# Performance work log

Hardware: AMD Instinct MI355X
Metric: run time of the kernel (lower is better)

## Reference

```python
import jax, jax.numpy as jnp
import numpy as np

N, HID, EMB, T_ENC, T_DEC = 10000, 64, 64, 12, 12


def setup_inputs() -> dict:
    key = jax.random.key(0)
    ks = jax.random.split(key, 16)
    s = 0.05  # small init scale (xavier-ish)
    inputs = jax.random.normal(ks[0], (N, T_ENC), dtype=jnp.float32)
    targets = jax.random.normal(ks[1], (N, T_DEC), dtype=jnp.float32)
    a = jax.random.uniform(ks[2], (N, N), dtype=jnp.float32)
    adj_matrix = a / a.sum(axis=1, keepdims=True)  # row-normalized dense learned adjacency
    D_e = EMB + HID  # encoder cell input dim (embedded input + hidden)
    D_d = 1 + HID    # decoder cell input dim (scalar input + hidden)
    return {
        "inputs": inputs,
        "targets": targets,
        "adj_matrix": adj_matrix,
        "W_emb": jax.random.normal(ks[3], (1, EMB)) * s,
        "b_emb": jnp.full((EMB,), 0.1, dtype=jnp.float32),
        "Wg_e": jax.random.normal(ks[4], (3 * D_e, 2 * HID)) * s,
        "bg_e": jnp.zeros((2 * HID,), jnp.float32),
        "Wc_e": jax.random.normal(ks[5], (3 * D_e, HID)) * s,
        "bc_e": jnp.zeros((HID,), jnp.float32),
        "Wg_d": jax.random.normal(ks[6], (3 * D_d, 2 * HID)) * s,
        "bg_d": jnp.zeros((2 * HID,), jnp.float32),
        "Wc_d": jax.random.normal(ks[7], (3 * D_d, HID)) * s,
        "bc_d": jnp.zeros((HID,), jnp.float32),
        "W_pred": jax.random.normal(ks[8], (HID, 1)) * s,
        "b_pred": jnp.full((1,), 0.1, dtype=jnp.float32),
    }


def _gconv(adj, inp, W, b):
    # Chebyshev-style diffusion with max_diffusion_step = 2: [x0, A x0, 2A(A x0) - x0]
    x1 = adj @ inp
    x2 = 2.0 * (adj @ x1) - inp
    return jnp.concatenate([inp, x1, x2], axis=-1) @ W + b


def _dcgru_cell(adj, x, h, Wg, bg, Wc, bc):
    ru = jax.nn.sigmoid(_gconv(adj, jnp.concatenate([x, h], axis=-1), Wg, bg))
    r, u = jnp.split(ru, 2, axis=-1)
    c = jnp.tanh(_gconv(adj, jnp.concatenate([x, r * h], axis=-1), Wc, bc))
    return u * h + (1.0 - u) * c


def reference(inputs, targets, adj_matrix, W_emb, b_emb, Wg_e, bg_e, Wc_e, bc_e,
              Wg_d, bg_d, Wc_d, bc_d, W_pred, b_pred):
    adj = adj_matrix

    def enc_step(h, xt):  # xt: (N,)
        e = xt[:, None] @ W_emb + b_emb  # (N, EMB)
        return _dcgru_cell(adj, e, h, Wg_e, bg_e, Wc_e, bc_e), None

    h0 = jnp.zeros((N, HID), dtype=inputs.dtype)
    h_enc, _ = jax.lax.scan(enc_step, h0, inputs.T)

    def dec_step(carry, _):
        h, x = carry  # x: (N, 1) previous prediction (go symbol = zeros)
        h = _dcgru_cell(adj, x, h, Wg_d, bg_d, Wc_d, bc_d)
        out = h @ W_pred + b_pred  # (N, 1)
        return (h, out), out[:, 0]

    go = jnp.zeros((N, 1), dtype=inputs.dtype)
    _, outs = jax.lax.scan(dec_step, (h_enc, go), None, length=T_DEC)
    return outs.T  # (N, T_DEC)
```

## Files before the change

kernel.cpp:

```cpp
#include <hip/hip_runtime.h>


typedef unsigned short u16;
typedef __attribute__((ext_vector_type(8))) short short8;
typedef __attribute__((ext_vector_type(8))) unsigned short u16x8;
typedef __attribute__((ext_vector_type(4))) unsigned short u16x4;
typedef __attribute__((ext_vector_type(4))) float f32x4;

#define NN 10000
#define P 10112
#define KPAD 10048
#define SPLITS 13
#define KSPLIT 768
#define PLANE 808960

__device__ __forceinline__ u16 f2bf(float f) {
  unsigned u = __float_as_uint(f);
  unsigned r = (u + 0x7FFFu + ((u >> 16) & 1u)) >> 16;
  return (u16)r;
}
__device__ __forceinline__ float bf2f(u16 v) {
  return __uint_as_float((unsigned)v << 16);
}

__device__ __forceinline__ void load_lds16(const void* g, void* l) {
  __builtin_amdgcn_global_load_lds(
      (__attribute__((address_space(1))) void*)(void*)g,
      (__attribute__((address_space(3))) void*)l, 16, 0, 0);
}

__global__ __launch_bounds__(256) void cvt_bf16(const float* __restrict__ a,
                                                u16* __restrict__ o) {
  long i = ((long)blockIdx.x * 256 + threadIdx.x) * 8;
  if (i >= 100000000L) return;
  float4 x = *(const float4*)(a + i);
  float4 y = *(const float4*)(a + i + 4);
  u16x8 v;
  v[0]=f2bf(x.x); v[1]=f2bf(x.y); v[2]=f2bf(x.z); v[3]=f2bf(x.w);
  v[4]=f2bf(y.x); v[5]=f2bf(y.y); v[6]=f2bf(y.z); v[7]=f2bf(y.w);
  *(u16x8*)(o + i) = v;
}

__global__ __launch_bounds__(256) void prep_in(const float* __restrict__ in,
                                               u16* __restrict__ Htin) {
  int m = blockIdx.x * 256 + threadIdx.x;
  int c = blockIdx.y;
  if (m >= NN) return;
  Htin[(size_t)c * P + m] = f2bf(in[(size_t)m * 12 + c]);
}

__global__ void build_w_enc(const float* __restrict__ W, const float* __restrict__ wemb,
    const float* __restrict__ bemb, const float* __restrict__ bsrc, int nout,
    u16* __restrict__ Wt, float* __restrict__ biasout) {
  int j = blockIdx.x, k = threadIdx.x;
  float v = 0.f;
  if (k < 64)        v = W[(64 + k) * nout + j] - W[(320 + k) * nout + j];
  else if (k < 128)  v = W[(192 + (k - 64)) * nout + j];
  else if (k < 192)  v = 2.f * W[(320 + (k - 128)) * nout + j];
  else if (k == 192) { float s = 0; for (int i = 0; i < 64; i++) s += wemb[i] * (W[i*nout+j] - W[(256+i)*nout+j]); v = s; }
  else if (k == 193) { float s = 0; for (int i = 0; i < 64; i++) s += wemb[i] * W[(128+i)*nout+j]; v = s; }
  else if (k == 194) { float s = 0; for (int i = 0; i < 64; i++) s += wemb[i] * W[(256+i)*nout+j]; v = 2.f * s; }
  Wt[j * 256 + k] = f2bf(v);
  if (k == 195) {
    float bb = bsrc[j];
    for (int i = 0; i < 64; i++) bb += bemb[i] * (W[i*nout+j] + W[(128+i)*nout+j] + W[(256+i)*nout+j]);
    biasout[j] = bb;
  }
}

__global__ void build_w_dec(const float* __restrict__ W, int nout, u16* __restrict__ Wt) {
  int j = blockIdx.x, k = threadIdx.x;
  float v = 0.f;
  if (k < 64)        v = W[(1 + k) * nout + j] - W[(131 + k) * nout + j];
  else if (k < 128)  v = W[(66 + (k - 64)) * nout + j];
  else if (k < 192)  v = 2.f * W[(131 + (k - 128)) * nout + j];
  else if (k == 192) v = W[0 * nout + j] - W[130 * nout + j];
  else if (k == 193) v = W[65 * nout + j];
  else if (k == 194) v = 2.f * W[130 * nout + j];
  Wt[j * 256 + k] = f2bf(v);
}

template <int NT>
__global__ __launch_bounds__(256) void gemm_bt_t(
    const u16* __restrict__ A, const u16* __restrict__ Ht,
    u16* __restrict__ PT) {
  __shared__ u16 Al[2][128 * 64];
  __shared__ u16 Bl[2][NT * 16 * 64];
  int tid = threadIdx.x;
  int wave = tid >> 6, lane = tid & 63, ml = lane & 15, q = lane >> 4;
  int row0 = blockIdx.x * 128;
  int kb = blockIdx.y * KSPLIT;
  int ke = (blockIdx.y == SPLITS - 1) ? KPAD : kb + KSPLIT;
  int nch = (ke - kb) >> 6;
  f32x4 acc[2][NT] = {};
  int r8 = tid >> 3, c8 = tid & 7;
  int csw = c8 ^ (r8 & 7);

  auto stageA = [&](int buf, int k0) {
    int kch = k0 + csw * 8;
    kch = kch > 9992 ? 9992 : kch;
#pragma unroll
    for (int is = 0; is < 4; is++) {
      int row = row0 + is * 32 + r8;
      row = row > 9999 ? 9999 : row;
      load_lds16(A + (size_t)row * NN + kch,
                 (u16*)&Al[buf][0] + is * 2048 + wave * 512);
    }
  };
  auto stageB = [&](int buf, int k0) {
    int kk = k0 + csw * 8;
    if constexpr (NT >= 4) {
#pragma unroll
      for (int is = 0; is < 2; is++)
        load_lds16(Ht + (size_t)(is * 32 + r8) * P + kk,
                   (u16*)&Bl[buf][0] + is * 2048 + wave * 512);
    }
    if constexpr (NT == 5) {
      if (wave < 2)
        load_lds16(Ht + (size_t)(64 + r8) * P + kk,
                   (u16*)&Bl[buf][0] + 4096 + wave * 512);
    }
    if constexpr (NT == 1) {
      if (wave < 2)
        load_lds16(Ht + (size_t)r8 * P + kk,
                   (u16*)&Bl[buf][0] + wave * 512);
    }
  };

  stageA(0, kb);
  stageB(0, kb);
  for (int c = 0; c < nch; c++) {
    int buf = c & 1;
    if (c + 1 < nch) {
      stageA(buf ^ 1, kb + (c + 1) * 64);
      stageB(buf ^ 1, kb + (c + 1) * 64);
      __builtin_amdgcn_sched_barrier(0);
      if constexpr (NT == 5) {
        if (wave < 2) asm volatile("s_waitcnt vmcnt(7)" ::: "memory");
        else          asm volatile("s_waitcnt vmcnt(6)" ::: "memory");
      } else if constexpr (NT == 4) {
        asm volatile("s_waitcnt vmcnt(6)" ::: "memory");
      } else {
        if (wave < 2) asm volatile("s_waitcnt vmcnt(5)" ::: "memory");
        else          asm volatile("s_waitcnt vmcnt(4)" ::: "memory");
      }
    } else {
      asm volatile("s_waitcnt vmcnt(0)" ::: "memory");
    }
    __builtin_amdgcn_sched_barrier(0);
    __builtin_amdgcn_s_barrier();
    __builtin_amdgcn_sched_barrier(0);
#pragma unroll
    for (int kh = 0; kh < 2; kh++) {
      int s = ((kh * 4 + q) ^ (ml & 7)) * 8;
      short8 a0 = *(const short8*)(&Al[buf][0] + (wave * 32 + ml) * 64 + s);
      short8 a1 = *(const short8*)(&Al[buf][0] + (wave * 32 + 16 + ml) * 64 + s);
#pragma unroll
      for (int nt = 0; nt < NT; nt++) {
        short8 b = *(const short8*)(&Bl[buf][0] + (nt * 16 + ml) * 64 + s);
        acc[0][nt] = __builtin_amdgcn_mfma_f32_16x16x32_bf16(a0, b, acc[0][nt], 0, 0, 0);
        acc[1][nt] = __builtin_amdgcn_mfma_f32_16x16x32_bf16(a1, b, acc[1][nt], 0, 0, 0);
      }
    }
    __builtin_amdgcn_sched_barrier(0);
    __builtin_amdgcn_s_barrier();
    __builtin_amdgcn_sched_barrier(0);
  }
  u16* Pp = PT + (size_t)blockIdx.y * PLANE;
#pragma unroll
  for (int mt = 0; mt < 2; mt++)
#pragma unroll
    for (int nt = 0; nt < NT; nt++) {
      int j = nt * 16 + ml;
      int m = row0 + wave * 32 + mt * 16 + q * 4;
      u16x4 pk;
#pragma unroll
      for (int i = 0; i < 4; i++) pk[i] = f2bf(acc[mt][nt][i]);
      *(u16x4*)(Pp + (size_t)j * P + m) = pk;
    }
}

__global__ __launch_bounds__(256) void red(const u16* __restrict__ PT,
                                           int ncols, u16* __restrict__ T) {
  int nch = ncols * 1264;
  for (int cid = blockIdx.x * 256 + threadIdx.x; cid < nch; cid += gridDim.x * 256) {
    int c = cid / 1264;
    int mb8 = (cid - c * 1264) * 8;
    size_t base = (size_t)c * P + mb8;
    float a[8] = {};
#pragma unroll
    for (int s = 0; s < SPLITS; s++) {
      u16x8 v = *(const u16x8*)(PT + (size_t)s * PLANE + base);
#pragma unroll
      for (int i = 0; i < 8; i++) a[i] += bf2f(v[i]);
    }
    u16x8 o;
#pragma unroll
    for (int i = 0; i < 8; i++) o[i] = (mb8 >= NN) ? (u16)0 : f2bf(a[i]);
    *(u16x8*)(T + base) = o;
  }
}

__global__ __launch_bounds__(256) void cellmm(
    const u16* __restrict__ src0row,
    const u16* __restrict__ T1, const u16* __restrict__ T2,
    const u16* __restrict__ sc0, const u16* __restrict__ sc1,
    const u16* __restrict__ sc2,
    u16* __restrict__ sdec0, u16* __restrict__ sdec1,
    const u16* __restrict__ Wt, const float* __restrict__ bias,
    int ntiles, int mode,
    const float* __restrict__ hx,
    float* __restrict__ ubuf,
    float* __restrict__ hxout,
    u16* __restrict__ rowout,
    u16* __restrict__ htout) {
  __shared__ u16 Al[128 * 64];
  __shared__ u16 Wl[128 * 64];
  int tid = threadIdx.x;
  int wave = tid >> 6, lane = tid & 63, ml = lane & 15, q = lane >> 4;
  int m0 = blockIdx.x * 128;
  int r8 = tid >> 3, c8 = tid & 7;
  int csw = c8 ^ (r8 & 7);
  f32x4 acc[2][8] = {};
  for (int kc = 0; kc < 4; kc++) {
    if (kc == 0) {
#pragma unroll
      for (int is = 0; is < 4; is++) {
        int row = m0 + is * 32 + r8;
        load_lds16(src0row + (size_t)row * 64 + csw * 8,
                   (u16*)Al + is * 2048 + wave * 512);
      }
    } else if (kc < 3) {
      const u16* Ts = (kc == 1) ? T1 : T2;
      int c = tid >> 2;
      int mo = (tid & 3) * 32;
      const u16* sp = Ts + (size_t)c * P + m0 + mo;
      u16x8 v0 = *(const u16x8*)(sp);
      u16x8 v1 = *(const u16x8*)(sp + 8);
      u16x8 v2 = *(const u16x8*)(sp + 16);
      u16x8 v3 = *(const u16x8*)(sp + 24);
#pragma unroll
      for (int i = 0; i < 8; i++) {
        int cs = c ^ (i << 3);
        Al[(mo + i) * 64 + cs]      = v0[i];
        Al[(mo + 8 + i) * 64 + cs]  = v1[i];
        Al[(mo + 16 + i) * 64 + cs] = v2[i];
        Al[(mo + 24 + i) * 64 + cs] = v3[i];
      }
    } else {
      int r = tid >> 1, half = tid & 1;
      int m = m0 + r;
      int x = (r & 7) << 3;
      u16* rowp = Al + r * 64;
      if (half == 0) {
        u16 a = sc0[m], b = sc1[m], cc = sc2[m];
        rowp[0 ^ x] = a; rowp[1 ^ x] = b; rowp[2 ^ x] = cc;
#pragma unroll
        for (int jj = 3; jj < 32; jj++) rowp[jj ^ x] = 0;
        if (sdec0) { sdec0[m] = b; sdec1[m] = cc; }
      } else {
#pragma unroll
        for (int jj = 32; jj < 64; jj++) rowp[jj ^ x] = 0;
      }
    }
    int wiss = ntiles >> 1;
    for (int is = 0; is < wiss; is++) {
      int jr = is * 32 + r8;
      load_lds16(Wt + (size_t)jr * 256 + kc * 64 + csw * 8,
                 (u16*)Wl + is * 2048 + wave * 512);
    }
    __syncthreads();
#pragma unroll
    for (int kh = 0; kh < 2; kh++) {
      int s = ((kh * 4 + q) ^ (ml & 7)) * 8;
      short8 a0 = *(const short8*)(Al + (wave * 32 + ml) * 64 + s);
      short8 a1 = *(const short8*)(Al + (wave * 32 + 16 + ml) * 64 + s);
#pragma unroll
      for (int nt = 0; nt < 8; nt++) {
        if (nt < ntiles) {
          short8 b = *(const short8*)(Wl + (nt * 16 + ml) * 64 + s);
          acc[0][nt] = __builtin_amdgcn_mfma_f32_16x16x32_bf16(a0, b, acc[0][nt], 0, 0, 0);
          acc[1][nt] = __builtin_amdgcn_mfma_f32_16x16x32_bf16(a1, b, acc[1][nt], 0, 0, 0);
        }
      }
    }
    __syncthreads();
  }
#pragma unroll
  for (int mt = 0; mt < 2; mt++)
#pragma unroll
    for (int nt = 0; nt < 8; nt++)
      if (nt < ntiles) {
        int j = nt * 16 + ml;
        int mb = m0 + wave * 32 + mt * 16 + q * 4;
        u16x4 pk;
        if (mode == 0) {
          if (j < 64) {
#pragma unroll
            for (int i = 0; i < 4; i++) {
              int m = mb + i;
              float g = acc[mt][nt][i] + bias[j];
              float s = 1.f / (1.f + __expf(-g));
              float rv = s * hx[(size_t)m * 64 + j];
              rowout[(size_t)m * 64 + j] = f2bf(rv);
              pk[i] = f2bf(rv);
            }
            if (mb < NN) *(u16x4*)(htout + (size_t)j * P + mb) = pk;
          } else {
#pragma unroll
            for (int i = 0; i < 4; i++) {
              int m = mb + i;
              float g = acc[mt][nt][i] + bias[j];
              ubuf[(size_t)m * 64 + (j - 64)] = 1.f / (1.f + __expf(-g));
            }
          }
        } else {
#pragma unroll
          for (int i = 0; i < 4; i++) {
            int m = mb + i;
            float g = acc[mt][nt][i] + bias[j];
            float cc = 1.f - 2.f / (__expf(2.f * g) + 1.f);
            float uu = ubuf[(size_t)m * 64 + j];
            float hv = hx[(size_t)m * 64 + j];
            float hn = uu * hv + (1.f - uu) * cc;
            hxout[(size_t)m * 64 + j] = hn;
            rowout[(size_t)m * 64 + j] = f2bf(hn);
            pk[i] = f2bf(hn);
          }
          if (mb < NN) *(u16x4*)(htout + (size_t)j * P + mb) = pk;
        }
      }
}

__global__ __launch_bounds__(256) void pred_k(const float* __restrict__ hx,
    const float* __restrict__ Wp, const float* __restrict__ bp,
    float* __restrict__ out, u16* __restrict__ xrow, u16* __restrict__ Ht1,
    int t) {
  int m = blockIdx.x * 256 + threadIdx.x;
  if (m >= P) return;
  const float* h = hx + (size_t)m * 64;
  float s = bp[0];
#pragma unroll
  for (int j = 0; j < 64; j += 4) {
    float4 f = *(const float4*)(h + j);
    s += f.x * Wp[j] + f.y * Wp[j + 1] + f.z * Wp[j + 2] + f.w * Wp[j + 3];
  }
  u16 sb = f2bf(s);
  xrow[m] = sb;
  if (m < NN) {
    Ht1[(size_t)64 * P + m] = sb;
    out[(size_t)m * 12 + t] = s;
  }
}

extern "C" void kernel_launch(void* const* d_in, const int* in_sizes, int n_in,
                              void* d_out, int out_size, void* d_ws, size_t ws_size,
                              hipStream_t stream) {
  const float* inputs = (const float*)d_in[0];
  const float* adj    = (const float*)d_in[2];
  const float* W_emb  = (const float*)d_in[3];
  const float* b_emb  = (const float*)d_in[4];
  const float* Wg_e   = (const float*)d_in[5];
  const float* bg_e   = (const float*)d_in[6];
  const float* Wc_e   = (const float*)d_in[7];
  const float* bc_e   = (const float*)d_in[8];
  const float* Wg_d   = (const float*)d_in[9];
  const float* bg_d   = (const float*)d_in[10];
  const float* Wc_d   = (const float*)d_in[11];
  const float* bc_d   = (const float*)d_in[12];
  const float* W_pred = (const float*)d_in[13];
  const float* b_pred = (const float*)d_in[14];
  float* out = (float*)d_out;
  char* ws = (char*)d_ws;

  size_t off = 0;
  auto alloc = [&](size_t bytes) -> void* {
    void* p = ws + off;
    off += (bytes + 511) & ~(size_t)511;
    return p;
  };
  u16*   A16    = (u16*)  alloc(200000000ULL);
  u16*   PT1    = (u16*)  alloc((size_t)SPLITS * PLANE * 2);
  u16*   PT2    = (u16*)  alloc((size_t)SPLITS * PLANE * 2);
  u16*   Ht1    = (u16*)  alloc((size_t)80 * P * 2);
  u16*   T1     = (u16*)  alloc((size_t)80 * P * 2);
  u16*   T2     = (u16*)  alloc((size_t)80 * P * 2);
  u16*   HtR    = (u16*)  alloc((size_t)64 * P * 2);
  u16*   Htin   = (u16*)  alloc((size_t)16 * P * 2);
  u16*   Ts1    = (u16*)  alloc((size_t)16 * P * 2);
  u16*   Ts2    = (u16*)  alloc((size_t)16 * P * 2);
  float* hx     = (float*)alloc((size_t)P * 64 * 4);
  float* ub     = (float*)alloc((size_t)P * 64 * 4);
  u16*   hxrow  = (u16*)  alloc((size_t)P * 64 * 2);
  u16*   rhrow  = (u16*)  alloc((size_t)P * 64 * 2);
  u16*   xrow   = (u16*)  alloc((size_t)P * 2);
  u16*   sdec   = (u16*)  alloc((size_t)2 * P * 2);
  u16*   Wt_eg  = (u16*)  alloc(128 * 256 * 2);
  u16*   Wt_ec  = (u16*)  alloc(64 * 256 * 2);
  u16*   Wt_dg  = (u16*)  alloc(128 * 256 * 2);
  u16*   Wt_dc  = (u16*)  alloc(64 * 256 * 2);
  float* bias_eg= (float*)alloc(128 * 4);
  float* bias_ec= (float*)alloc(64 * 4);
  if (off > ws_size) return;

  hipMemsetAsync(Ht1, 0, (size_t)80 * P * 2, stream);
  hipMemsetAsync(HtR, 0, (size_t)64 * P * 2, stream);
  hipMemsetAsync(Htin, 0, (size_t)16 * P * 2, stream);
  hipMemsetAsync(hx, 0, (size_t)P * 64 * 4, stream);
  hipMemsetAsync(hxrow, 0, (size_t)P * 64 * 2, stream);
  hipMemsetAsync(xrow, 0, (size_t)P * 2, stream);

  cvt_bf16<<<48829, 256, 0, stream>>>(adj, A16);
  prep_in<<<dim3(40, 12), 256, 0, stream>>>(inputs, Htin);
  build_w_enc<<<128, 256, 0, stream>>>(Wg_e, W_emb, b_emb, bg_e, 128, Wt_eg, bias_eg);
  build_w_enc<<<64, 256, 0, stream>>>(Wc_e, W_emb, b_emb, bc_e, 64, Wt_ec, bias_ec);
  build_w_dec<<<128, 256, 0, stream>>>(Wg_d, 128, Wt_dg);
  build_w_dec<<<64, 256, 0, stream>>>(Wc_d, 64, Wt_dc);

  dim3 ggrid(79, SPLITS);
  gemm_bt_t<1><<<ggrid, 256, 0, stream>>>(A16, Htin, PT1);
  red<<<256, 256, 0, stream>>>(PT1, 16, Ts1);
  gemm_bt_t<1><<<ggrid, 256, 0, stream>>>(A16, Ts1, PT2);
  red<<<256, 256, 0, stream>>>(PT2, 16, Ts2);

  for (int t = 0; t < 12; t++) {
    gemm_bt_t<4><<<ggrid, 256, 0, stream>>>(A16, Ht1, PT1);
    red<<<256, 256, 0, stream>>>(PT1, 64, T1);
    gemm_bt_t<4><<<ggrid, 256, 0, stream>>>(A16, T1, PT2);
    red<<<256, 256, 0, stream>>>(PT2, 64, T2);
    cellmm<<<79, 256, 0, stream>>>(hxrow, T1, T2,
        Htin + (size_t)t * P, Ts1 + (size_t)t * P, Ts2 + (size_t)t * P,
        (u16*)nullptr, (u16*)nullptr, Wt_eg, bias_eg, 8, 0,
        hx, ub, (float*)nullptr, rhrow, HtR);
    gemm_bt_t<4><<<ggrid, 256, 0, stream>>>(A16, HtR, PT1);
    red<<<256, 256, 0, stream>>>(PT1, 64, T1);
    gemm_bt_t<4><<<ggrid, 256, 0, stream>>>(A16, T1, PT2);
    red<<<256, 256, 0, stream>>>(PT2, 64, T2);
    cellmm<<<79, 256, 0, stream>>>(rhrow, T1, T2,
        Htin + (size_t)t * P, Ts1 + (size_t)t * P, Ts2 + (size_t)t * P,
        (u16*)nullptr, (u16*)nullptr, Wt_ec, bias_ec, 4, 1,
        hx, ub, hx, hxrow, Ht1);
  }
  for (int t = 0; t < 12; t++) {
    gemm_bt_t<5><<<ggrid, 256, 0, stream>>>(A16, Ht1, PT1);
    red<<<256, 256, 0, stream>>>(PT1, 80, T1);
    gemm_bt_t<5><<<ggrid, 256, 0, stream>>>(A16, T1, PT2);
    red<<<256, 256, 0, stream>>>(PT2, 80, T2);
    cellmm<<<79, 256, 0, stream>>>(hxrow, T1, T2,
        xrow, T1 + (size_t)64 * P, T2 + (size_t)64 * P,
        sdec, sdec + P, Wt_dg, bg_d, 8, 0,
        hx, ub, (float*)nullptr, rhrow, HtR);
    gemm_bt_t<4><<<ggrid, 256, 0, stream>>>(A16, HtR, PT1);
    red<<<256, 256, 0, stream>>>(PT1, 64, T1);
    gemm_bt_t<4><<<ggrid, 256, 0, stream>>>(A16, T1, PT2);
    red<<<256, 256, 0, stream>>>(PT2, 64, T2);
    cellmm<<<79, 256, 0, stream>>>(rhrow, T1, T2,
        xrow, sdec, sdec + P,
        (u16*)nullptr, (u16*)nullptr, Wt_dc, bc_d, 4, 1,
        hx, ub, hx, hxrow, Ht1);
    pred_k<<<40, 256, 0, stream>>>(hx, W_pred, b_pred, out, xrow, Ht1, t);
  }
}
```

Baseline: 6.283 ms.

## Pre-pack adjacency into swizzled tile-contiguous bf16 blocks for GEMM staging

Replaces the flat bf16 conversion of the adjacency with a packing kernel that writes each 128x64 tile contiguously, already in the swizzled LDS order and zero-padded. The GEMM then stages A with purely contiguous 16-byte loads, with no row/column clamping or strided row accesses. This removes scattered row-stride reads and the per-load address math in every GEMM of the 48 recurrent diffusions. The reduction kernels' grid sizes are also changed to scale with the number of output rows. Risks are a more complex pack kernel and correctness depending on the packed layout matching the GEMM's LDS layout.

```diff
diff --git a/kernel.cpp b/kernel.cpp
--- a/kernel.cpp
+++ b/kernel.cpp
@@ -10,6 +10,7 @@
 #define NN 10000
 #define P 10112
 #define KPAD 10048
+#define NCHUNK 157
 #define SPLITS 13
 #define KSPLIT 768
 #define PLANE 808960
@@ -29,16 +30,25 @@
       (__attribute__((address_space(3))) void*)l, 16, 0, 0);
 }
 
-__global__ __launch_bounds__(256) void cvt_bf16(const float* __restrict__ a,
-                                                u16* __restrict__ o) {
-  long i = ((long)blockIdx.x * 256 + threadIdx.x) * 8;
-  if (i >= 100000000L) return;
-  float4 x = *(const float4*)(a + i);
-  float4 y = *(const float4*)(a + i + 4);
-  u16x8 v;
-  v[0]=f2bf(x.x); v[1]=f2bf(x.y); v[2]=f2bf(x.z); v[3]=f2bf(x.w);
-  v[4]=f2bf(y.x); v[5]=f2bf(y.y); v[6]=f2bf(y.z); v[7]=f2bf(y.w);
-  *(u16x8*)(o + i) = v;
+__global__ __launch_bounds__(256) void pack_a(const float* __restrict__ a,
+                                              u16* __restrict__ A2) {
+  int bx = blockIdx.x, g = blockIdx.y;
+  size_t tb = ((size_t)bx * NCHUNK + g) << 13;
+#pragma unroll
+  for (int q = 0; q < 4; q++) {
+    int s = q * 256 + threadIdx.x;
+    int is = s >> 8, w = (s >> 6) & 3, lane = s & 63;
+    int row = bx * 128 + is * 32 + 8 * w + (lane >> 3);
+    int k = g * 64 + (((lane & 7) ^ ((lane >> 3) & 7)) << 3);
+    u16x8 v = {};
+    if (row < NN && k < NN) {
+      float4 x = *(const float4*)(a + (size_t)row * NN + k);
+      float4 y = *(const float4*)(a + (size_t)row * NN + k + 4);
+      v[0]=f2bf(x.x); v[1]=f2bf(x.y); v[2]=f2bf(x.z); v[3]=f2bf(x.w);
+      v[4]=f2bf(y.x); v[5]=f2bf(y.y); v[6]=f2bf(y.z); v[7]=f2bf(y.w);
+    }
+    *(u16x8*)(A2 + tb + (size_t)s * 8) = v;
+  }
 }
 
 __global__ __launch_bounds__(256) void prep_in(const float* __restrict__ in,
@@ -82,33 +92,30 @@
 
 template <int NT>
 __global__ __launch_bounds__(256) void gemm_bt_t(
-    const u16* __restrict__ A, const u16* __restrict__ Ht,
+    const u16* __restrict__ A2, const u16* __restrict__ Ht,
     u16* __restrict__ PT) {
   __shared__ u16 Al[2][128 * 64];
   __shared__ u16 Bl[2][NT * 16 * 64];
   int tid = threadIdx.x;
   int wave = tid >> 6, lane = tid & 63, ml = lane & 15, q = lane >> 4;
   int row0 = blockIdx.x * 128;
-  int kb = blockIdx.y * KSPLIT;
-  int ke = (blockIdx.y == SPLITS - 1) ? KPAD : kb + KSPLIT;
-  int nch = (ke - kb) >> 6;
+  int g0 = blockIdx.y * 12;
+  int nch = (blockIdx.y == SPLITS - 1) ? 13 : 12;
   f32x4 acc[2][NT] = {};
   int r8 = tid >> 3, c8 = tid & 7;
   int csw = c8 ^ (r8 & 7);
 
-  auto stageA = [&](int buf, int k0) {
-    int kch = k0 + csw * 8;
-    kch = kch > 9992 ? 9992 : kch;
-#pragma unroll
-    for (int is = 0; is < 4; is++) {
-      int row = row0 + is * 32 + r8;
-      row = row > 9999 ? 9999 : row;
-      load_lds16(A + (size_t)row * NN + kch,
-                 (u16*)&Al[buf][0] + is * 2048 + wave * 512);
-    }
+  const u16* Abase = A2 + (((size_t)blockIdx.x * NCHUNK + g0) << 13)
+                        + wave * 512 + (size_t)lane * 8;
+
+  auto stageA = [&](int buf, int c) {
+    const u16* src = Abase + ((size_t)c << 13);
+#pragma unroll
+    for (int is = 0; is < 4; is++)
+      load_lds16(src + is * 2048, (u16*)&Al[buf][0] + is * 2048 + wave * 512);
   };
-  auto stageB = [&](int buf, int k0) {
-    int kk = k0 + csw * 8;
+  auto stageB = [&](int buf, int c) {
+    int kk = (g0 + c) * 64 + csw * 8;
     if constexpr (NT >= 4) {
 #pragma unroll
       for (int is = 0; is < 2; is++)
@@ -127,13 +134,13 @@
     }
   };
 
-  stageA(0, kb);
-  stageB(0, kb);
+  stageA(0, 0);
+  stageB(0, 0);
   for (int c = 0; c < nch; c++) {
     int buf = c & 1;
     if (c + 1 < nch) {
-      stageA(buf ^ 1, kb + (c + 1) * 64);
-      stageB(buf ^ 1, kb + (c + 1) * 64);
+      stageA(buf ^ 1, c + 1);
+      stageB(buf ^ 1, c + 1);
       __builtin_amdgcn_sched_barrier(0);
       if constexpr (NT == 5) {
         if (wave < 2) asm volatile("s_waitcnt vmcnt(7)" ::: "memory");
@@ -379,7 +386,7 @@
     off += (bytes + 511) & ~(size_t)511;
     return p;
   };
-  u16*   A16    = (u16*)  alloc(200000000ULL);
+  u16*   A2     = (u16*)  alloc((size_t)79 * NCHUNK * 8192 * 2);
   u16*   PT1    = (u16*)  alloc((size_t)SPLITS * PLANE * 2);
   u16*   PT2    = (u16*)  alloc((size_t)SPLITS * PLANE * 2);
   u16*   Ht1    = (u16*)  alloc((size_t)80 * P * 2);
@@ -410,7 +417,7 @@
   hipMemsetAsync(hxrow, 0, (size_t)P * 64 * 2, stream);
   hipMemsetAsync(xrow, 0, (size_t)P * 2, stream);
 
-  cvt_bf16<<<48829, 256, 0, stream>>>(adj, A16);
+  pack_a<<<dim3(79, NCHUNK), 256, 0, stream>>>(adj, A2);
   prep_in<<<dim3(40, 12), 256, 0, stream>>>(inputs, Htin);
   build_w_enc<<<128, 256, 0, stream>>>(Wg_e, W_emb, b_emb, bg_e, 128, Wt_eg, bias_eg);
   build_w_enc<<<64, 256, 0, stream>>>(Wc_e, W_emb, b_emb, bc_e, 64, Wt_ec, bias_ec);
@@ -418,42 +425,42 @@
   build_w_dec<<<64, 256, 0, stream>>>(Wc_d, 64, Wt_dc);
 
   dim3 ggrid(79, SPLITS);
-  gemm_bt_t<1><<<ggrid, 256, 0, stream>>>(A16, Htin, PT1);
-  red<<<256, 256, 0, stream>>>(PT1, 16, Ts1);
-  gemm_bt_t<1><<<ggrid, 256, 0, stream>>>(A16, Ts1, PT2);
-  red<<<256, 256, 0, stream>>>(PT2, 16, Ts2);
+  gemm_bt_t<1><<<ggrid, 256, 0, stream>>>(A2, Htin, PT1);
+  red<<<79, 256, 0, stream>>>(PT1, 16, Ts1);
+  gemm_bt_t<1><<<ggrid, 256, 0, stream>>>(A2, Ts1, PT2);
+  red<<<79, 256, 0, stream>>>(PT2, 16, Ts2);
 
   for (int t = 0; t < 12; t++) {
-    gemm_bt_t<4><<<ggrid, 256, 0, stream>>>(A16, Ht1, PT1);
-    red<<<256, 256, 0, stream>>>(PT1, 64, T1);
-    gemm_bt_t<4><<<ggrid, 256, 0, stream>>>(A16, T1, PT2);
-    red<<<256, 256, 0, stream>>>(PT2, 64, T2);
+    gemm_bt_t<4><<<ggrid, 256, 0, stream>>>(A2, Ht1, PT1);
+    red<<<316, 256, 0, stream>>>(PT1, 64, T1);
+    gemm_bt_t<4><<<ggrid, 256, 0, stream>>>(A2, T1, PT2);
+    red<<<316, 256, 0, stream>>>(PT2, 64, T2);
     cellmm<<<79, 256, 0, stream>>>(hxrow, T1, T2,
         Htin + (size_t)t * P, Ts1 + (size_t)t * P, Ts2 + (size_t)t * P,
         (u16*)nullptr, (u16*)nullptr, Wt_eg, bias_eg, 8, 0,
         hx, ub, (float*)nullptr, rhrow, HtR);
-    gemm_bt_t<4><<<ggrid, 256, 0, stream>>>(A16, HtR, PT1);
-    red<<<256, 256, 0, stream>>>(PT1, 64, T1);
-    gemm_bt_t<4><<<ggrid, 256, 0, stream>>>(A16, T1, PT2);
-    red<<<256, 256, 0, stream>>>(PT2, 64, T2);
+    gemm_bt_t<4><<<ggrid, 256, 0, stream>>>(A2, HtR, PT1);
+    red<<<316, 256, 0, stream>>>(PT1, 64, T1);
+    gemm_bt_t<4><<<ggrid, 256, 0, stream>>>(A2, T1, PT2);
+    red<<<316, 256, 0, stream>>>(PT2, 64, T2);
     cellmm<<<79, 256, 0, stream>>>(rhrow, T1, T2,
         Htin + (size_t)t * P, Ts1 + (size_t)t * P, Ts2 + (size_t)t * P,
         (u16*)nullptr, (u16*)nullptr, Wt_ec, bias_ec, 4, 1,
         hx, ub, hx, hxrow, Ht1);
   }
   for (int t = 0; t < 12; t++) {
-    gemm_bt_t<5><<<ggrid, 256, 0, stream>>>(A16, Ht1, PT1);
-    red<<<256, 256, 0, stream>>>(PT1, 80, T1);
-    gemm_bt_t<5><<<ggrid, 256, 0, stream>>>(A16, T1, PT2);
-    red<<<256, 256, 0, stream>>>(PT2, 80, T2);
+    gemm_bt_t<5><<<ggrid, 256, 0, stream>>>(A2, Ht1, PT1);
+    red<<<395, 256, 0, stream>>>(PT1, 80, T1);
+    gemm_bt_t<5><<<ggrid, 256, 0, stream>>>(A2, T1, PT2);
+    red<<<395, 256, 0, stream>>>(PT2, 80, T2);
     cellmm<<<79, 256, 0, stream>>>(hxrow, T1, T2,
         xrow, T1 + (size_t)64 * P, T2 + (size_t)64 * P,
         sdec, sdec + P, Wt_dg, bg_d, 8, 0,
         hx, ub, (float*)nullptr, rhrow, HtR);
-    gemm_bt_t<4><<<ggrid, 256, 0, stream>>>(A16, HtR, PT1);
-    red<<<256, 256, 0, stream>>>(PT1, 64, T1);
-    gemm_bt_t<4><<<ggrid, 256, 0, stream>>>(A16, T1, PT2);
-    red<<<256, 256, 0, stream>>>(PT2, 64, T2);
+    gemm_bt_t<4><<<ggrid, 256, 0, stream>>>(A2, HtR, PT1);
+    red<<<316, 256, 0, stream>>>(PT1, 64, T1);
+    gemm_bt_t<4><<<ggrid, 256, 0, stream>>>(A2, T1, PT2);
+    red<<<316, 256, 0, stream>>>(PT2, 64, T2);
     cellmm<<<79, 256, 0, stream>>>(rhrow, T1, T2,
         xrow, sdec, sdec + P,
         (u16*)nullptr, (u16*)nullptr, Wt_dc, bc_d, 4, 1,
```

New measurement: 5.713 ms. 9.1% less time.
